# Optimization experiments

Measured on AMD Instinct MI355X. Metric: run time of the kernel, lower is better.

## Reference

```python
import jax, jax.numpy as jnp
import numpy as np

MARGIN = 1.0   # TripletLoss(margin) init arg
EPS = 1e-6     # torch F.pairwise_distance eps used by nn.TripletMarginLoss
INF = 1e9

N, D_EMB, N_CLASSES = 8192, 1024, 128


def setup_inputs() -> dict:
    key = jax.random.key(0)
    k1, k2 = jax.random.split(key)
    embeddings = jax.random.normal(k1, (N, D_EMB), dtype=jnp.float32)
    target = jax.random.randint(k2, (N,), 0, N_CLASSES, dtype=jnp.int64 if jax.config.jax_enable_x64 else jnp.int32)
    return {"embeddings": embeddings, "target": target}


def _mine_and_loss(embeddings, target):
    # Vectorized, deterministic equivalent of the per-anchor random mining loop:
    # full pairwise L2 distance matrix via a GEMM (compute-bound core).
    sq = jnp.sum(embeddings * embeddings, axis=1)                      # [N]
    d2 = sq[:, None] + sq[None, :] - 2.0 * (embeddings @ embeddings.T)  # [N, N]
    Dm = jnp.sqrt(jnp.maximum(d2, 0.0))                                 # [N, N]

    same = target[:, None] == target[None, :]
    eye = jnp.eye(target.shape[0], dtype=bool)
    pos_mask = same & ~eye          # valid positives (same class, not self)
    neg_mask = ~same                # valid negatives (different class)

    # Positive: hardest (farthest) same-class sample (deterministic stand-in
    # for the original's random positive draw).
    pos_scores = jnp.where(pos_mask, Dm, -INF)
    pos_idx = jnp.argmax(pos_scores, axis=1)                           # [N]
    d_p = jnp.max(pos_scores, axis=1)                                  # [N]

    # Negative: semi-hard (d_p < d_n < d_p + margin), pick the closest such
    # negative; if none exists, fall back to the overall hardest (min-dist)
    # negative -- mirrors the loop's early-break vs. min_dist fallback.
    semi = neg_mask & (Dm > d_p[:, None]) & (Dm < (d_p + MARGIN)[:, None])
    has_semi = jnp.any(semi, axis=1)
    neg_semi = jnp.argmin(jnp.where(semi, Dm, INF), axis=1)
    neg_hard = jnp.argmin(jnp.where(neg_mask, Dm, INF), axis=1)
    neg_idx = jnp.where(has_semi, neg_semi, neg_hard)                  # [N]

    # nn.TripletMarginLoss(margin, p=2): mean(relu(d(a,p) - d(a,n) + margin))
    # with torch's pairwise_distance eps added to the difference.
    a = embeddings
    p = embeddings[pos_idx]
    n = embeddings[neg_idx]
    dp = jnp.sqrt(jnp.sum((a - p + EPS) ** 2, axis=1))
    dn = jnp.sqrt(jnp.sum((a - n + EPS) ** 2, axis=1))
    return jnp.mean(jax.nn.relu(dp - dn + MARGIN))


def reference(embeddings, target):
    return _mine_and_loss(embeddings, target)
```

## Files before the change

### kernel.cpp

```cpp
#include <hip/hip_runtime.h>
#include <hip/hip_bf16.h>

#define N 8192
#define D 1024
#define MARGIN 1.0f
#define TSTR 132

typedef __attribute__((ext_vector_type(8))) short bf16x8;
typedef __attribute__((ext_vector_type(4))) float f32x4;
typedef __attribute__((ext_vector_type(8))) _Float16 f16x8;
typedef __attribute__((ext_vector_type(4))) _Float16 f16x4;
typedef __attribute__((ext_vector_type(8))) unsigned short u16x8;

__device__ inline unsigned short f2bf(float x) {
    unsigned u = __float_as_uint(x);
    unsigned r = (u + 0x7FFFu + ((u >> 16) & 1u)) >> 16;
    return (unsigned short)r;
}

__device__ inline float h2f(unsigned hb) {
    return (float)__builtin_bit_cast(_Float16, (unsigned short)(hb & 0xFFFFu));
}

__device__ inline void tri_decode(int l, int& a, int& b) {
    int bb = (int)((sqrtf(8.0f * (float)l + 1.0f) - 1.0f) * 0.5f);
    while ((bb + 1) * (bb + 2) / 2 <= l) ++bb;
    while (bb * (bb + 1) / 2 > l) --bb;
    b = bb;
    a = l - bb * (bb + 1) / 2;
}

__global__ __launch_bounds__(256) void prep_kernel(const float* __restrict__ E,
                                                   const int* __restrict__ target,
                                                   unsigned short* __restrict__ Ebf,
                                                   float* __restrict__ sq,
                                                   unsigned char* __restrict__ cls,
                                                   unsigned* __restrict__ P,
                                                   unsigned* __restrict__ Nn,
                                                   unsigned* __restrict__ S,
                                                   float* __restrict__ out) {
    const int r = blockIdx.x;
    const int tid = threadIdx.x;
    if (r < 32) {
        const int idx = r * 256 + tid;
        cls[idx] = (unsigned char)target[idx];
        P[idx] = 0u;
        Nn[idx] = 0xFFFFFFFFu;
        S[idx] = 0xFFFFFFFFu;
        if (idx == 0) out[0] = 0.0f;
    }
    const float4 v = ((const float4*)(E + (size_t)r * D))[tid];
    ushort4 o;
    o.x = f2bf(v.x); o.y = f2bf(v.y); o.z = f2bf(v.z); o.w = f2bf(v.w);
    ((ushort4*)(Ebf + (size_t)r * D))[tid] = o;
    float s = v.x * v.x + v.y * v.y + v.z * v.z + v.w * v.w;
    for (int off = 32; off > 0; off >>= 1) s += __shfl_down(s, off);
    __shared__ float red[4];
    const int lane = tid & 63, wave = tid >> 6;
    if (lane == 0) red[wave] = s;
    __syncthreads();
    if (tid == 0) sq[r] = red[0] + red[1] + red[2] + red[3];
}

__global__ __launch_bounds__(256) void gemm_kernel(const unsigned short* __restrict__ E,
                                                   const float* __restrict__ sq,
                                                   _Float16* __restrict__ D2h) {
    __shared__ char smem[128 * TSTR * 2];
    unsigned short* As = (unsigned short*)smem;
    unsigned short* Bs = (unsigned short*)(smem + 8192);
    _Float16* Ts = (_Float16*)smem;

    const int tid = threadIdx.x;
    const int lane = tid & 63;
    const int wave = tid >> 6;
    const int wm = wave & 1, wn = wave >> 1;

    int bx, by;
    tri_decode(blockIdx.x, bx, by);
    const int rm = by * 128;
    const int cn = bx * 128;

    const int srow = tid >> 2;
    const int rot_s = (srow >> 1) & 3;
    const int scol = (((tid & 3) + rot_s) & 3) * 8;

    const unsigned short* gA = E + (size_t)(rm + srow) * D + scol;
    const unsigned short* gB = E + (size_t)(cn + srow) * D + scol;

    f32x4 acc[4][4] = {};

    const int mr = lane & 15;
    const int kq2 = ((((lane >> 4)) - ((mr >> 1) & 3)) & 3) * 8;

    for (int k0 = 0; k0 < D; k0 += 32) {
        __builtin_amdgcn_global_load_lds(
            (const __attribute__((address_space(1))) unsigned int*)(gA + k0),
            (__attribute__((address_space(3))) unsigned int*)((char*)As + wave * 1024), 16, 0, 0);
        __builtin_amdgcn_global_load_lds(
            (const __attribute__((address_space(1))) unsigned int*)(gA + (size_t)64 * D + k0),
            (__attribute__((address_space(3))) unsigned int*)((char*)As + 4096 + wave * 1024), 16, 0, 0);
        __builtin_amdgcn_global_load_lds(
            (const __attribute__((address_space(1))) unsigned int*)(gB + k0),
            (__attribute__((address_space(3))) unsigned int*)((char*)Bs + wave * 1024), 16, 0, 0);
        __builtin_amdgcn_global_load_lds(
            (const __attribute__((address_space(1))) unsigned int*)(gB + (size_t)64 * D + k0),
            (__attribute__((address_space(3))) unsigned int*)((char*)Bs + 4096 + wave * 1024), 16, 0, 0);
        __syncthreads();

        bf16x8 af[4], bfr[4];
#pragma unroll
        for (int mi = 0; mi < 4; ++mi)
            af[mi] = *(const bf16x8*)(As + (wm * 64 + mi * 16 + mr) * 32 + kq2);
#pragma unroll
        for (int ni = 0; ni < 4; ++ni)
            bfr[ni] = *(const bf16x8*)(Bs + (wn * 64 + ni * 16 + mr) * 32 + kq2);
#pragma unroll
        for (int mi = 0; mi < 4; ++mi)
#pragma unroll
            for (int ni = 0; ni < 4; ++ni)
                acc[mi][ni] = __builtin_amdgcn_mfma_f32_16x16x32_bf16(af[mi], bfr[ni], acc[mi][ni], 0, 0, 0);
        __syncthreads();
    }

    const int crow = (lane >> 4) * 4;
    const int ccol = lane & 15;
    float sqj[4];
#pragma unroll
    for (int ni = 0; ni < 4; ++ni)
        sqj[ni] = sq[cn + wn * 64 + ni * 16 + ccol];
#pragma unroll
    for (int mi = 0; mi < 4; ++mi) {
        const int lrow = wm * 64 + mi * 16 + crow;
        const int i0 = rm + lrow;
        float sqi[4];
#pragma unroll
        for (int r = 0; r < 4; ++r) sqi[r] = sq[i0 + r];
#pragma unroll
        for (int ni = 0; ni < 4; ++ni) {
            const int lcol = wn * 64 + ni * 16 + ccol;
            f16x4 tv;
#pragma unroll
            for (int r = 0; r < 4; ++r) {
                float d2 = fmaxf(sqi[r] + sqj[ni] - 2.0f * acc[mi][ni][r], 0.0f);
                tv[r] = (_Float16)d2;
            }
            *(f16x4*)(Ts + (size_t)lcol * TSTR + lrow) = tv;
        }
    }
    __syncthreads();
#pragma unroll
    for (int it = 0; it < 8; ++it) {
        const int rt = it * 16 + (tid >> 4);
        const int seg = tid & 15;
        f16x4 v0 = *(const f16x4*)(Ts + (size_t)rt * TSTR + seg * 8);
        f16x4 v1 = *(const f16x4*)(Ts + (size_t)rt * TSTR + seg * 8 + 4);
        f16x8 v = __builtin_shufflevector(v0, v1, 0, 1, 2, 3, 4, 5, 6, 7);
        *(f16x8*)(D2h + (size_t)(cn + rt) * N + rm + seg * 8) = v;
    }
}

__global__ __launch_bounds__(256) void mineA_kernel(const _Float16* __restrict__ D2h,
                                                    const unsigned char* __restrict__ cls,
                                                    unsigned* __restrict__ P,
                                                    unsigned* __restrict__ Nn) {
    __shared__ unsigned char clsA_l[128], clsB_l[128];
    __shared__ unsigned short colP_l[4][128], colN_l[4][128];
    const int tid = threadIdx.x;
    const int lane = tid & 63, wave = tid >> 6;
    int a, b;
    tri_decode(blockIdx.x, a, b);
    if (tid < 128) clsA_l[tid] = cls[a * 128 + tid];
    else           clsB_l[tid - 128] = cls[b * 128 + (tid - 128)];
    __syncthreads();

    const int cg = tid & 15;
    const int rg = tid >> 4;
    const unsigned long long c8 = *(const unsigned long long*)(clsB_l + cg * 8);
    const unsigned short* g = (const unsigned short*)D2h + (size_t)(a * 128) * N + b * 128 + cg * 8;
    const bool offdiag = (a != b);

    unsigned cp[8], cnn[8];
#pragma unroll
    for (int e = 0; e < 8; ++e) { cp[e] = 0u; cnn[e] = 0xFFFFu; }

#pragma unroll
    for (int k = 0; k < 8; ++k) {
        const int r = k * 16 + rg;
        const unsigned rc = clsA_l[r];
        const u16x8 v = *(const u16x8*)(g + (size_t)r * N);
        unsigned rp = 0u, rn = 0xFFFFu;
#pragma unroll
        for (int e = 0; e < 8; ++e) {
            const unsigned hb = v[e];
            const bool s = (((unsigned)(c8 >> (8 * e)) & 0xFFu) == rc);
            rp = max(rp, s ? hb : 0u);
            rn = min(rn, s ? 0xFFFFu : hb);
            cp[e] = max(cp[e], s ? hb : 0u);
            cnn[e] = min(cnn[e], s ? 0xFFFFu : hb);
        }
#pragma unroll
        for (int m = 1; m < 16; m <<= 1) {
            rp = max(rp, (unsigned)__shfl_xor((int)rp, m));
            rn = min(rn, (unsigned)__shfl_xor((int)rn, m));
        }
        if (cg == 0) {
            atomicMax(&P[a * 128 + r], rp);
            atomicMin(&Nn[a * 128 + r], rn);
        }
    }
    if (offdiag) {
#pragma unroll
        for (int e = 0; e < 8; ++e) {
#pragma unroll
            for (int m = 16; m < 64; m <<= 1) {
                cp[e] = max(cp[e], (unsigned)__shfl_xor((int)cp[e], m));
                cnn[e] = min(cnn[e], (unsigned)__shfl_xor((int)cnn[e], m));
            }
        }
        if (lane < 16) {
#pragma unroll
            for (int e = 0; e < 8; ++e) {
                colP_l[wave][cg * 8 + e] = (unsigned short)cp[e];
                colN_l[wave][cg * 8 + e] = (unsigned short)cnn[e];
            }
        }
        __syncthreads();
        if (tid < 128) {
            const unsigned pm = max(max((unsigned)colP_l[0][tid], (unsigned)colP_l[1][tid]),
                                    max((unsigned)colP_l[2][tid], (unsigned)colP_l[3][tid]));
            const unsigned nm = min(min((unsigned)colN_l[0][tid], (unsigned)colN_l[1][tid]),
                                    min((unsigned)colN_l[2][tid], (unsigned)colN_l[3][tid]));
            atomicMax(&P[b * 128 + tid], pm);
            atomicMin(&Nn[b * 128 + tid], nm);
        }
    }
}

__global__ __launch_bounds__(256) void mineB_kernel(const _Float16* __restrict__ D2h,
                                                    const unsigned* __restrict__ P,
                                                    unsigned* __restrict__ S) {
    __shared__ unsigned short lobA_l[128], lobB_l[128];
    __shared__ unsigned short colS_l[4][128];
    const int tid = threadIdx.x;
    const int lane = tid & 63, wave = tid >> 6;
    int a, b;
    tri_decode(blockIdx.x, a, b);
    if (tid < 128) lobA_l[tid] = (unsigned short)P[a * 128 + tid];
    else           lobB_l[tid - 128] = (unsigned short)P[b * 128 + (tid - 128)];
    __syncthreads();

    const int cg = tid & 15;
    const int rg = tid >> 4;
    unsigned lb[8];
#pragma unroll
    for (int e = 0; e < 8; ++e) lb[e] = lobB_l[cg * 8 + e];
    const unsigned short* g = (const unsigned short*)D2h + (size_t)(a * 128) * N + b * 128 + cg * 8;
    const bool offdiag = (a != b);

    unsigned sc[8];
#pragma unroll
    for (int e = 0; e < 8; ++e) sc[e] = 0xFFFFu;

#pragma unroll
    for (int k = 0; k < 8; ++k) {
        const int r = k * 16 + rg;
        const unsigned lr = lobA_l[r];
        const u16x8 v = *(const u16x8*)(g + (size_t)r * N);
        unsigned sr = 0xFFFFu;
#pragma unroll
        for (int e = 0; e < 8; ++e) {
            const unsigned hb = v[e];
            sr = min(sr, hb > lr ? hb : 0xFFFFu);
            sc[e] = min(sc[e], hb > lb[e] ? hb : 0xFFFFu);
        }
#pragma unroll
        for (int m = 1; m < 16; m <<= 1)
            sr = min(sr, (unsigned)__shfl_xor((int)sr, m));
        if (cg == 0)
            atomicMin(&S[a * 128 + r], sr);
    }
    if (offdiag) {
#pragma unroll
        for (int e = 0; e < 8; ++e) {
#pragma unroll
            for (int m = 16; m < 64; m <<= 1)
                sc[e] = min(sc[e], (unsigned)__shfl_xor((int)sc[e], m));
        }
        if (lane < 16) {
#pragma unroll
            for (int e = 0; e < 8; ++e)
                colS_l[wave][cg * 8 + e] = (unsigned short)sc[e];
        }
        __syncthreads();
        if (tid < 128) {
            const unsigned sm = min(min((unsigned)colS_l[0][tid], (unsigned)colS_l[1][tid]),
                                    min((unsigned)colS_l[2][tid], (unsigned)colS_l[3][tid]));
            atomicMin(&S[b * 128 + tid], sm);
        }
    }
}

__global__ __launch_bounds__(256) void foldB_kernel(const unsigned* __restrict__ P,
                                                    const unsigned* __restrict__ Nn,
                                                    const unsigned* __restrict__ S,
                                                    float* __restrict__ out) {
    const int tid = threadIdx.x;
    const int i = blockIdx.x * 256 + tid;
    const float lo = h2f(P[i]);
    const float dp = sqrtf(lo);
    const float hw = dp + MARGIN;
    const float hi = hw * hw;
    const float smv = h2f(S[i]);
    const float dn2 = (smv < hi) ? smv : h2f(Nn[i]);
    float loss = fmaxf(dp - sqrtf(dn2) + MARGIN, 0.0f);
    for (int off = 32; off > 0; off >>= 1) loss += __shfl_down(loss, off);
    __shared__ float red[4];
    const int lane = tid & 63, wave = tid >> 6;
    if (lane == 0) red[wave] = loss;
    __syncthreads();
    if (tid == 0)
        atomicAdd(out, (red[0] + red[1] + red[2] + red[3]) * (1.0f / N));
}

extern "C" void kernel_launch(void* const* d_in, const int* in_sizes, int n_in,
                              void* d_out, int out_size, void* d_ws, size_t ws_size,
                              hipStream_t stream) {
    const float* E = (const float*)d_in[0];
    const int* target = (const int*)d_in[1];
    float* out = (float*)d_out;
    char* ws = (char*)d_ws;

    unsigned short* Ebf = (unsigned short*)ws;
    float* sq           = (float*)(ws + (size_t)16777216);
    unsigned char* cls  = (unsigned char*)(ws + (size_t)16809984);
    unsigned* P         = (unsigned*)(ws + (size_t)16842752);
    unsigned* Nn        = (unsigned*)(ws + (size_t)16875520);
    unsigned* S         = (unsigned*)(ws + (size_t)16908288);
    _Float16* D2h       = (_Float16*)(ws + (size_t)16941056);

    prep_kernel<<<N, 256, 0, stream>>>(E, target, Ebf, sq, cls, P, Nn, S, out);
    gemm_kernel<<<2080, 256, 0, stream>>>(Ebf, sq, D2h);
    mineA_kernel<<<2080, 256, 0, stream>>>(D2h, cls, P, Nn);
    mineB_kernel<<<2080, 256, 0, stream>>>(D2h, P, S);
    foldB_kernel<<<N / 256, 256, 0, stream>>>(P, Nn, S, out);
}
```

Baseline: 212.1 us.

## Fuse positive/hard-negative mining into GEMM epilogue and pack distance tiles

The first mining pass (hardest positive and hardest negative per row and column) now runs inside the GEMM epilogue on the register-resident fp16 distances, with per-block reductions through shared memory and atomics. This removes the separate mineA kernel and its full read of the distance matrix. Distance tiles are also stored contiguously per block instead of in the row-major N×N layout, so mineB reads them as one coalesced chunk. The cost is more epilogue work and register pressure in the GEMM, which could lower its occupancy.

```diff
diff --git a/kernel.cpp b/kernel.cpp
--- a/kernel.cpp
+++ b/kernel.cpp
@@ -64,11 +64,17 @@
 
 __global__ __launch_bounds__(256) void gemm_kernel(const unsigned short* __restrict__ E,
                                                    const float* __restrict__ sq,
-                                                   _Float16* __restrict__ D2h) {
+                                                   const unsigned char* __restrict__ cls,
+                                                   _Float16* __restrict__ D2pk,
+                                                   unsigned* __restrict__ P,
+                                                   unsigned* __restrict__ Nn) {
     __shared__ char smem[128 * TSTR * 2];
     unsigned short* As = (unsigned short*)smem;
     unsigned short* Bs = (unsigned short*)(smem + 8192);
     _Float16* Ts = (_Float16*)smem;
+    __shared__ unsigned char clr_l[128], clc_l[128];
+    __shared__ unsigned short rowP_l[256], rowN_l[256];
+    __shared__ unsigned short colP_l[256], colN_l[256];
 
     const int tid = threadIdx.x;
     const int lane = tid & 63;
@@ -79,6 +85,9 @@
     tri_decode(blockIdx.x, bx, by);
     const int rm = by * 128;
     const int cn = bx * 128;
+
+    if (tid < 128) clr_l[tid] = cls[rm + tid];
+    else           clc_l[tid - 128] = cls[cn + tid - 128];
 
     const int srow = tid >> 2;
     const int rot_s = (srow >> 1) & 3;
@@ -122,19 +131,31 @@
         __syncthreads();
     }
 
-    const int crow = (lane >> 4) * 4;
+    const int q = lane >> 4;
     const int ccol = lane & 15;
-    float sqj[4];
-#pragma unroll
-    for (int ni = 0; ni < 4; ++ni)
-        sqj[ni] = sq[cn + wn * 64 + ni * 16 + ccol];
+    const bool offdiag = (bx != by);
+
+    float sqj[4]; unsigned cj[4];
+#pragma unroll
+    for (int ni = 0; ni < 4; ++ni) {
+        const int lcol = wn * 64 + ni * 16 + ccol;
+        sqj[ni] = sq[cn + lcol];
+        cj[ni] = clc_l[lcol];
+    }
+
+    unsigned cp[4], cnn[4];
+#pragma unroll
+    for (int ni = 0; ni < 4; ++ni) { cp[ni] = 0u; cnn[ni] = 0xFFFFu; }
+
 #pragma unroll
     for (int mi = 0; mi < 4; ++mi) {
-        const int lrow = wm * 64 + mi * 16 + crow;
-        const int i0 = rm + lrow;
-        float sqi[4];
-#pragma unroll
-        for (int r = 0; r < 4; ++r) sqi[r] = sq[i0 + r];
+        const int lrow0 = wm * 64 + mi * 16 + q * 4;
+        float sqi[4]; unsigned ci[4];
+#pragma unroll
+        for (int r = 0; r < 4; ++r) { sqi[r] = sq[rm + lrow0 + r]; ci[r] = clr_l[lrow0 + r]; }
+        unsigned rp[4], rn[4];
+#pragma unroll
+        for (int r = 0; r < 4; ++r) { rp[r] = 0u; rn[r] = 0xFFFFu; }
 #pragma unroll
         for (int ni = 0; ni < 4; ++ni) {
             const int lcol = wn * 64 + ni * 16 + ccol;
@@ -142,12 +163,58 @@
 #pragma unroll
             for (int r = 0; r < 4; ++r) {
                 float d2 = fmaxf(sqi[r] + sqj[ni] - 2.0f * acc[mi][ni][r], 0.0f);
-                tv[r] = (_Float16)d2;
+                _Float16 h = (_Float16)d2;
+                tv[r] = h;
+                const unsigned hb = (unsigned)__builtin_bit_cast(unsigned short, h);
+                const bool s = (ci[r] == cj[ni]);
+                rp[r] = max(rp[r], s ? hb : 0u);
+                rn[r] = min(rn[r], s ? 0xFFFFu : hb);
+                cp[ni] = max(cp[ni], s ? hb : 0u);
+                cnn[ni] = min(cnn[ni], s ? 0xFFFFu : hb);
             }
-            *(f16x4*)(Ts + (size_t)lcol * TSTR + lrow) = tv;
+            *(f16x4*)(Ts + (size_t)lcol * TSTR + lrow0) = tv;
+        }
+#pragma unroll
+        for (int r = 0; r < 4; ++r) {
+#pragma unroll
+            for (int m = 1; m < 16; m <<= 1) {
+                rp[r] = max(rp[r], (unsigned)__shfl_xor((int)rp[r], m));
+                rn[r] = min(rn[r], (unsigned)__shfl_xor((int)rn[r], m));
+            }
+            if (ccol == 0) {
+                rowP_l[(lrow0 + r) * 2 + wn] = (unsigned short)rp[r];
+                rowN_l[(lrow0 + r) * 2 + wn] = (unsigned short)rn[r];
+            }
+        }
+    }
+#pragma unroll
+    for (int ni = 0; ni < 4; ++ni) {
+#pragma unroll
+        for (int m = 16; m < 64; m <<= 1) {
+            cp[ni] = max(cp[ni], (unsigned)__shfl_xor((int)cp[ni], m));
+            cnn[ni] = min(cnn[ni], (unsigned)__shfl_xor((int)cnn[ni], m));
+        }
+        if (q == 0) {
+            const int lcol = wn * 64 + ni * 16 + ccol;
+            colP_l[lcol * 2 + wm] = (unsigned short)cp[ni];
+            colN_l[lcol * 2 + wm] = (unsigned short)cnn[ni];
         }
     }
     __syncthreads();
+
+    if (tid < 128) {
+        const unsigned pm = max((unsigned)rowP_l[tid * 2], (unsigned)rowP_l[tid * 2 + 1]);
+        const unsigned nm = min((unsigned)rowN_l[tid * 2], (unsigned)rowN_l[tid * 2 + 1]);
+        atomicMax(&P[rm + tid], pm);
+        atomicMin(&Nn[rm + tid], nm);
+    } else if (offdiag) {
+        const int t = tid - 128;
+        const unsigned pm = max((unsigned)colP_l[t * 2], (unsigned)colP_l[t * 2 + 1]);
+        const unsigned nm = min((unsigned)colN_l[t * 2], (unsigned)colN_l[t * 2 + 1]);
+        atomicMax(&P[cn + t], pm);
+        atomicMin(&Nn[cn + t], nm);
+    }
+
 #pragma unroll
     for (int it = 0; it < 8; ++it) {
         const int rt = it * 16 + (tid >> 4);
@@ -155,88 +222,11 @@
         f16x4 v0 = *(const f16x4*)(Ts + (size_t)rt * TSTR + seg * 8);
         f16x4 v1 = *(const f16x4*)(Ts + (size_t)rt * TSTR + seg * 8 + 4);
         f16x8 v = __builtin_shufflevector(v0, v1, 0, 1, 2, 3, 4, 5, 6, 7);
-        *(f16x8*)(D2h + (size_t)(cn + rt) * N + rm + seg * 8) = v;
-    }
-}
-
-__global__ __launch_bounds__(256) void mineA_kernel(const _Float16* __restrict__ D2h,
-                                                    const unsigned char* __restrict__ cls,
-                                                    unsigned* __restrict__ P,
-                                                    unsigned* __restrict__ Nn) {
-    __shared__ unsigned char clsA_l[128], clsB_l[128];
-    __shared__ unsigned short colP_l[4][128], colN_l[4][128];
-    const int tid = threadIdx.x;
-    const int lane = tid & 63, wave = tid >> 6;
-    int a, b;
-    tri_decode(blockIdx.x, a, b);
-    if (tid < 128) clsA_l[tid] = cls[a * 128 + tid];
-    else           clsB_l[tid - 128] = cls[b * 128 + (tid - 128)];
-    __syncthreads();
-
-    const int cg = tid & 15;
-    const int rg = tid >> 4;
-    const unsigned long long c8 = *(const unsigned long long*)(clsB_l + cg * 8);
-    const unsigned short* g = (const unsigned short*)D2h + (size_t)(a * 128) * N + b * 128 + cg * 8;
-    const bool offdiag = (a != b);
-
-    unsigned cp[8], cnn[8];
-#pragma unroll
-    for (int e = 0; e < 8; ++e) { cp[e] = 0u; cnn[e] = 0xFFFFu; }
-
-#pragma unroll
-    for (int k = 0; k < 8; ++k) {
-        const int r = k * 16 + rg;
-        const unsigned rc = clsA_l[r];
-        const u16x8 v = *(const u16x8*)(g + (size_t)r * N);
-        unsigned rp = 0u, rn = 0xFFFFu;
-#pragma unroll
-        for (int e = 0; e < 8; ++e) {
-            const unsigned hb = v[e];
-            const bool s = (((unsigned)(c8 >> (8 * e)) & 0xFFu) == rc);
-            rp = max(rp, s ? hb : 0u);
-            rn = min(rn, s ? 0xFFFFu : hb);
-            cp[e] = max(cp[e], s ? hb : 0u);
-            cnn[e] = min(cnn[e], s ? 0xFFFFu : hb);
-        }
-#pragma unroll
-        for (int m = 1; m < 16; m <<= 1) {
-            rp = max(rp, (unsigned)__shfl_xor((int)rp, m));
-            rn = min(rn, (unsigned)__shfl_xor((int)rn, m));
-        }
-        if (cg == 0) {
-            atomicMax(&P[a * 128 + r], rp);
-            atomicMin(&Nn[a * 128 + r], rn);
-        }
-    }
-    if (offdiag) {
-#pragma unroll
-        for (int e = 0; e < 8; ++e) {
-#pragma unroll
-            for (int m = 16; m < 64; m <<= 1) {
-                cp[e] = max(cp[e], (unsigned)__shfl_xor((int)cp[e], m));
-                cnn[e] = min(cnn[e], (unsigned)__shfl_xor((int)cnn[e], m));
-            }
-        }
-        if (lane < 16) {
-#pragma unroll
-            for (int e = 0; e < 8; ++e) {
-                colP_l[wave][cg * 8 + e] = (unsigned short)cp[e];
-                colN_l[wave][cg * 8 + e] = (unsigned short)cnn[e];
-            }
-        }
-        __syncthreads();
-        if (tid < 128) {
-            const unsigned pm = max(max((unsigned)colP_l[0][tid], (unsigned)colP_l[1][tid]),
-                                    max((unsigned)colP_l[2][tid], (unsigned)colP_l[3][tid]));
-            const unsigned nm = min(min((unsigned)colN_l[0][tid], (unsigned)colN_l[1][tid]),
-                                    min((unsigned)colN_l[2][tid], (unsigned)colN_l[3][tid]));
-            atomicMax(&P[b * 128 + tid], pm);
-            atomicMin(&Nn[b * 128 + tid], nm);
-        }
-    }
-}
-
-__global__ __launch_bounds__(256) void mineB_kernel(const _Float16* __restrict__ D2h,
+        *(f16x8*)(D2pk + (size_t)blockIdx.x * 16384 + rt * 128 + seg * 8) = v;
+    }
+}
+
+__global__ __launch_bounds__(256) void mineB_kernel(const _Float16* __restrict__ D2pk,
                                                     const unsigned* __restrict__ P,
                                                     unsigned* __restrict__ S) {
     __shared__ unsigned short lobA_l[128], lobB_l[128];
@@ -250,11 +240,10 @@
     __syncthreads();
 
     const int cg = tid & 15;
-    const int rg = tid >> 4;
     unsigned lb[8];
 #pragma unroll
     for (int e = 0; e < 8; ++e) lb[e] = lobB_l[cg * 8 + e];
-    const unsigned short* g = (const unsigned short*)D2h + (size_t)(a * 128) * N + b * 128 + cg * 8;
+    const unsigned short* g = (const unsigned short*)D2pk + (size_t)blockIdx.x * 16384;
     const bool offdiag = (a != b);
 
     unsigned sc[8];
@@ -263,9 +252,9 @@
 
 #pragma unroll
     for (int k = 0; k < 8; ++k) {
-        const int r = k * 16 + rg;
+        const int r = k * 16 + (tid >> 4);
         const unsigned lr = lobA_l[r];
-        const u16x8 v = *(const u16x8*)(g + (size_t)r * N);
+        const u16x8 v = *(const u16x8*)(g + k * 2048 + tid * 8);
         unsigned sr = 0xFFFFu;
 #pragma unroll
         for (int e = 0; e < 8; ++e) {
@@ -336,11 +325,10 @@
     unsigned* P         = (unsigned*)(ws + (size_t)16842752);
     unsigned* Nn        = (unsigned*)(ws + (size_t)16875520);
     unsigned* S         = (unsigned*)(ws + (size_t)16908288);
-    _Float16* D2h       = (_Float16*)(ws + (size_t)16941056);
+    _Float16* D2pk      = (_Float16*)(ws + (size_t)16941056);
 
     prep_kernel<<<N, 256, 0, stream>>>(E, target, Ebf, sq, cls, P, Nn, S, out);
-    gemm_kernel<<<2080, 256, 0, stream>>>(Ebf, sq, D2h);
-    mineA_kernel<<<2080, 256, 0, stream>>>(D2h, cls, P, Nn);
-    mineB_kernel<<<2080, 256, 0, stream>>>(D2h, P, S);
+    gemm_kernel<<<2080, 256, 0, stream>>>(Ebf, sq, cls, D2pk, P, Nn);
+    mineB_kernel<<<2080, 256, 0, stream>>>(D2pk, P, S);
     foldB_kernel<<<N / 256, 256, 0, stream>>>(P, Nn, S, out);
 }
```

Result: slower. 231.0 us (+8.9%).

## Store distance tiles packed per block and replace atomics with partial buffers

Applied to the files above, without the earlier changes.

The GEMM now writes each 128x128 tile of the upper-triangular distance matrix contiguously per block instead of into a strided full N x N matrix, so the mining kernels read whole contiguous tiles. Per-row and per-column atomicMax/atomicMin on global arrays are replaced by writing per-tile partial maxima and minima into slab arrays (PR/PC/NR/NC/SR/SC). A new foldA kernel and an extended foldB kernel reduce those partials. This removes atomic contention and strided reads, at the cost of one extra kernel launch and extra partial-buffer traffic.

```diff
diff --git a/kernel.cpp b/kernel.cpp
--- a/kernel.cpp
+++ b/kernel.cpp
@@ -35,18 +35,12 @@
                                                    unsigned short* __restrict__ Ebf,
                                                    float* __restrict__ sq,
                                                    unsigned char* __restrict__ cls,
-                                                   unsigned* __restrict__ P,
-                                                   unsigned* __restrict__ Nn,
-                                                   unsigned* __restrict__ S,
                                                    float* __restrict__ out) {
     const int r = blockIdx.x;
     const int tid = threadIdx.x;
     if (r < 32) {
         const int idx = r * 256 + tid;
         cls[idx] = (unsigned char)target[idx];
-        P[idx] = 0u;
-        Nn[idx] = 0xFFFFFFFFu;
-        S[idx] = 0xFFFFFFFFu;
         if (idx == 0) out[0] = 0.0f;
     }
     const float4 v = ((const float4*)(E + (size_t)r * D))[tid];
@@ -64,7 +58,7 @@
 
 __global__ __launch_bounds__(256) void gemm_kernel(const unsigned short* __restrict__ E,
                                                    const float* __restrict__ sq,
-                                                   _Float16* __restrict__ D2h) {
+                                                   _Float16* __restrict__ D2pk) {
     __shared__ char smem[128 * TSTR * 2];
     unsigned short* As = (unsigned short*)smem;
     unsigned short* Bs = (unsigned short*)(smem + 8192);
@@ -155,15 +149,18 @@
         f16x4 v0 = *(const f16x4*)(Ts + (size_t)rt * TSTR + seg * 8);
         f16x4 v1 = *(const f16x4*)(Ts + (size_t)rt * TSTR + seg * 8 + 4);
         f16x8 v = __builtin_shufflevector(v0, v1, 0, 1, 2, 3, 4, 5, 6, 7);
-        *(f16x8*)(D2h + (size_t)(cn + rt) * N + rm + seg * 8) = v;
-    }
-}
-
-__global__ __launch_bounds__(256) void mineA_kernel(const _Float16* __restrict__ D2h,
+        *(f16x8*)(D2pk + (size_t)blockIdx.x * 16384 + rt * 128 + seg * 8) = v;
+    }
+}
+
+__global__ __launch_bounds__(256) void mineA_kernel(const _Float16* __restrict__ D2pk,
                                                     const unsigned char* __restrict__ cls,
-                                                    unsigned* __restrict__ P,
-                                                    unsigned* __restrict__ Nn) {
+                                                    unsigned short* __restrict__ PR,
+                                                    unsigned short* __restrict__ PC,
+                                                    unsigned short* __restrict__ NR,
+                                                    unsigned short* __restrict__ NC) {
     __shared__ unsigned char clsA_l[128], clsB_l[128];
+    __shared__ unsigned short rowP_l[128], rowN_l[128];
     __shared__ unsigned short colP_l[4][128], colN_l[4][128];
     const int tid = threadIdx.x;
     const int lane = tid & 63, wave = tid >> 6;
@@ -174,10 +171,8 @@
     __syncthreads();
 
     const int cg = tid & 15;
-    const int rg = tid >> 4;
     const unsigned long long c8 = *(const unsigned long long*)(clsB_l + cg * 8);
-    const unsigned short* g = (const unsigned short*)D2h + (size_t)(a * 128) * N + b * 128 + cg * 8;
-    const bool offdiag = (a != b);
+    const unsigned short* g = (const unsigned short*)D2pk + (size_t)blockIdx.x * 16384;
 
     unsigned cp[8], cnn[8];
 #pragma unroll
@@ -185,9 +180,9 @@
 
 #pragma unroll
     for (int k = 0; k < 8; ++k) {
-        const int r = k * 16 + rg;
+        const int r = k * 16 + (tid >> 4);
         const unsigned rc = clsA_l[r];
-        const u16x8 v = *(const u16x8*)(g + (size_t)r * N);
+        const u16x8 v = *(const u16x8*)(g + k * 2048 + tid * 8);
         unsigned rp = 0u, rn = 0xFFFFu;
 #pragma unroll
         for (int e = 0; e < 8; ++e) {
@@ -203,59 +198,77 @@
             rp = max(rp, (unsigned)__shfl_xor((int)rp, m));
             rn = min(rn, (unsigned)__shfl_xor((int)rn, m));
         }
-        if (cg == 0) {
-            atomicMax(&P[a * 128 + r], rp);
-            atomicMin(&Nn[a * 128 + r], rn);
-        }
-    }
-    if (offdiag) {
+        if (cg == 0) { rowP_l[r] = (unsigned short)rp; rowN_l[r] = (unsigned short)rn; }
+    }
+#pragma unroll
+    for (int e = 0; e < 8; ++e) {
+#pragma unroll
+        for (int m = 16; m < 64; m <<= 1) {
+            cp[e] = max(cp[e], (unsigned)__shfl_xor((int)cp[e], m));
+            cnn[e] = min(cnn[e], (unsigned)__shfl_xor((int)cnn[e], m));
+        }
+    }
+    if (lane < 16) {
 #pragma unroll
         for (int e = 0; e < 8; ++e) {
-#pragma unroll
-            for (int m = 16; m < 64; m <<= 1) {
-                cp[e] = max(cp[e], (unsigned)__shfl_xor((int)cp[e], m));
-                cnn[e] = min(cnn[e], (unsigned)__shfl_xor((int)cnn[e], m));
-            }
-        }
-        if (lane < 16) {
-#pragma unroll
-            for (int e = 0; e < 8; ++e) {
-                colP_l[wave][cg * 8 + e] = (unsigned short)cp[e];
-                colN_l[wave][cg * 8 + e] = (unsigned short)cnn[e];
-            }
-        }
-        __syncthreads();
-        if (tid < 128) {
-            const unsigned pm = max(max((unsigned)colP_l[0][tid], (unsigned)colP_l[1][tid]),
-                                    max((unsigned)colP_l[2][tid], (unsigned)colP_l[3][tid]));
-            const unsigned nm = min(min((unsigned)colN_l[0][tid], (unsigned)colN_l[1][tid]),
-                                    min((unsigned)colN_l[2][tid], (unsigned)colN_l[3][tid]));
-            atomicMax(&P[b * 128 + tid], pm);
-            atomicMin(&Nn[b * 128 + tid], nm);
-        }
-    }
-}
-
-__global__ __launch_bounds__(256) void mineB_kernel(const _Float16* __restrict__ D2h,
-                                                    const unsigned* __restrict__ P,
-                                                    unsigned* __restrict__ S) {
+            colP_l[wave][cg * 8 + e] = (unsigned short)cp[e];
+            colN_l[wave][cg * 8 + e] = (unsigned short)cnn[e];
+        }
+    }
+    __syncthreads();
+    if (tid < 128) {
+        PR[(size_t)b * N + a * 128 + tid] = rowP_l[tid];
+        NR[(size_t)b * N + a * 128 + tid] = rowN_l[tid];
+        const unsigned pm = max(max((unsigned)colP_l[0][tid], (unsigned)colP_l[1][tid]),
+                                max((unsigned)colP_l[2][tid], (unsigned)colP_l[3][tid]));
+        const unsigned nm = min(min((unsigned)colN_l[0][tid], (unsigned)colN_l[1][tid]),
+                                min((unsigned)colN_l[2][tid], (unsigned)colN_l[3][tid]));
+        PC[(size_t)a * N + b * 128 + tid] = (unsigned short)pm;
+        NC[(size_t)a * N + b * 128 + tid] = (unsigned short)nm;
+    }
+}
+
+__global__ __launch_bounds__(256) void foldA_kernel(const unsigned short* __restrict__ PR,
+                                                    const unsigned short* __restrict__ PC,
+                                                    const unsigned short* __restrict__ NR,
+                                                    const unsigned short* __restrict__ NC,
+                                                    unsigned short* __restrict__ P,
+                                                    unsigned short* __restrict__ Nn) {
+    const int i = blockIdx.x * 256 + threadIdx.x;
+    const int ai = i >> 7;
+    unsigned pm = 0u, nm = 0xFFFFu;
+    for (int s = ai; s < 64; ++s) {
+        pm = max(pm, (unsigned)PR[(size_t)s * N + i]);
+        nm = min(nm, (unsigned)NR[(size_t)s * N + i]);
+    }
+    for (int s = 0; s <= ai; ++s) {
+        pm = max(pm, (unsigned)PC[(size_t)s * N + i]);
+        nm = min(nm, (unsigned)NC[(size_t)s * N + i]);
+    }
+    P[i] = (unsigned short)pm;
+    Nn[i] = (unsigned short)nm;
+}
+
+__global__ __launch_bounds__(256) void mineB_kernel(const _Float16* __restrict__ D2pk,
+                                                    const unsigned short* __restrict__ P,
+                                                    unsigned short* __restrict__ SR,
+                                                    unsigned short* __restrict__ SC) {
     __shared__ unsigned short lobA_l[128], lobB_l[128];
+    __shared__ unsigned short rowS_l[128];
     __shared__ unsigned short colS_l[4][128];
     const int tid = threadIdx.x;
     const int lane = tid & 63, wave = tid >> 6;
     int a, b;
     tri_decode(blockIdx.x, a, b);
-    if (tid < 128) lobA_l[tid] = (unsigned short)P[a * 128 + tid];
-    else           lobB_l[tid - 128] = (unsigned short)P[b * 128 + (tid - 128)];
+    if (tid < 128) lobA_l[tid] = P[a * 128 + tid];
+    else           lobB_l[tid - 128] = P[b * 128 + (tid - 128)];
     __syncthreads();
 
     const int cg = tid & 15;
-    const int rg = tid >> 4;
     unsigned lb[8];
 #pragma unroll
     for (int e = 0; e < 8; ++e) lb[e] = lobB_l[cg * 8 + e];
-    const unsigned short* g = (const unsigned short*)D2h + (size_t)(a * 128) * N + b * 128 + cg * 8;
-    const bool offdiag = (a != b);
+    const unsigned short* g = (const unsigned short*)D2pk + (size_t)blockIdx.x * 16384;
 
     unsigned sc[8];
 #pragma unroll
@@ -263,9 +276,9 @@
 
 #pragma unroll
     for (int k = 0; k < 8; ++k) {
-        const int r = k * 16 + rg;
+        const int r = k * 16 + (tid >> 4);
         const unsigned lr = lobA_l[r];
-        const u16x8 v = *(const u16x8*)(g + (size_t)r * N);
+        const u16x8 v = *(const u16x8*)(g + k * 2048 + tid * 8);
         unsigned sr = 0xFFFFu;
 #pragma unroll
         for (int e = 0; e < 8; ++e) {
@@ -276,41 +289,44 @@
 #pragma unroll
         for (int m = 1; m < 16; m <<= 1)
             sr = min(sr, (unsigned)__shfl_xor((int)sr, m));
-        if (cg == 0)
-            atomicMin(&S[a * 128 + r], sr);
-    }
-    if (offdiag) {
-#pragma unroll
-        for (int e = 0; e < 8; ++e) {
-#pragma unroll
-            for (int m = 16; m < 64; m <<= 1)
-                sc[e] = min(sc[e], (unsigned)__shfl_xor((int)sc[e], m));
-        }
-        if (lane < 16) {
-#pragma unroll
-            for (int e = 0; e < 8; ++e)
-                colS_l[wave][cg * 8 + e] = (unsigned short)sc[e];
-        }
-        __syncthreads();
-        if (tid < 128) {
-            const unsigned sm = min(min((unsigned)colS_l[0][tid], (unsigned)colS_l[1][tid]),
-                                    min((unsigned)colS_l[2][tid], (unsigned)colS_l[3][tid]));
-            atomicMin(&S[b * 128 + tid], sm);
-        }
-    }
-}
-
-__global__ __launch_bounds__(256) void foldB_kernel(const unsigned* __restrict__ P,
-                                                    const unsigned* __restrict__ Nn,
-                                                    const unsigned* __restrict__ S,
+        if (cg == 0) rowS_l[r] = (unsigned short)sr;
+    }
+#pragma unroll
+    for (int e = 0; e < 8; ++e) {
+#pragma unroll
+        for (int m = 16; m < 64; m <<= 1)
+            sc[e] = min(sc[e], (unsigned)__shfl_xor((int)sc[e], m));
+    }
+    if (lane < 16) {
+#pragma unroll
+        for (int e = 0; e < 8; ++e)
+            colS_l[wave][cg * 8 + e] = (unsigned short)sc[e];
+    }
+    __syncthreads();
+    if (tid < 128) {
+        SR[(size_t)b * N + a * 128 + tid] = rowS_l[tid];
+        const unsigned sm = min(min((unsigned)colS_l[0][tid], (unsigned)colS_l[1][tid]),
+                                min((unsigned)colS_l[2][tid], (unsigned)colS_l[3][tid]));
+        SC[(size_t)a * N + b * 128 + tid] = (unsigned short)sm;
+    }
+}
+
+__global__ __launch_bounds__(256) void foldB_kernel(const unsigned short* __restrict__ SR,
+                                                    const unsigned short* __restrict__ SC,
+                                                    const unsigned short* __restrict__ P,
+                                                    const unsigned short* __restrict__ Nn,
                                                     float* __restrict__ out) {
     const int tid = threadIdx.x;
     const int i = blockIdx.x * 256 + tid;
+    const int ai = i >> 7;
+    unsigned sm = 0xFFFFu;
+    for (int s = ai; s < 64; ++s) sm = min(sm, (unsigned)SR[(size_t)s * N + i]);
+    for (int s = 0; s <= ai; ++s) sm = min(sm, (unsigned)SC[(size_t)s * N + i]);
     const float lo = h2f(P[i]);
     const float dp = sqrtf(lo);
     const float hw = dp + MARGIN;
     const float hi = hw * hw;
-    const float smv = h2f(S[i]);
+    const float smv = h2f(sm);
     const float dn2 = (smv < hi) ? smv : h2f(Nn[i]);
     float loss = fmaxf(dp - sqrtf(dn2) + MARGIN, 0.0f);
     for (int off = 32; off > 0; off >>= 1) loss += __shfl_down(loss, off);
@@ -333,14 +349,20 @@
     unsigned short* Ebf = (unsigned short*)ws;
     float* sq           = (float*)(ws + (size_t)16777216);
     unsigned char* cls  = (unsigned char*)(ws + (size_t)16809984);
-    unsigned* P         = (unsigned*)(ws + (size_t)16842752);
-    unsigned* Nn        = (unsigned*)(ws + (size_t)16875520);
-    unsigned* S         = (unsigned*)(ws + (size_t)16908288);
-    _Float16* D2h       = (_Float16*)(ws + (size_t)16941056);
-
-    prep_kernel<<<N, 256, 0, stream>>>(E, target, Ebf, sq, cls, P, Nn, S, out);
-    gemm_kernel<<<2080, 256, 0, stream>>>(Ebf, sq, D2h);
-    mineA_kernel<<<2080, 256, 0, stream>>>(D2h, cls, P, Nn);
-    mineB_kernel<<<2080, 256, 0, stream>>>(D2h, P, S);
-    foldB_kernel<<<N / 256, 256, 0, stream>>>(P, Nn, S, out);
-}
+    unsigned short* P   = (unsigned short*)(ws + (size_t)16842752);
+    unsigned short* Nn  = (unsigned short*)(ws + (size_t)16875520);
+    unsigned short* PR  = (unsigned short*)(ws + (size_t)16908288);
+    unsigned short* PC  = (unsigned short*)(ws + (size_t)17956864);
+    unsigned short* NR  = (unsigned short*)(ws + (size_t)19005440);
+    unsigned short* NC  = (unsigned short*)(ws + (size_t)20054016);
+    unsigned short* SR  = (unsigned short*)(ws + (size_t)21102592);
+    unsigned short* SC  = (unsigned short*)(ws + (size_t)22151168);
+    _Float16* D2pk      = (_Float16*)(ws + (size_t)23199744);
+
+    prep_kernel<<<N, 256, 0, stream>>>(E, target, Ebf, sq, cls, out);
+    gemm_kernel<<<2080, 256, 0, stream>>>(Ebf, sq, D2pk);
+    mineA_kernel<<<2080, 256, 0, stream>>>(D2pk, cls, PR, PC, NR, NC);
+    foldA_kernel<<<N / 256, 256, 0, stream>>>(PR, PC, NR, NC, P, Nn);
+    mineB_kernel<<<2080, 256, 0, stream>>>(D2pk, P, SR, SC);
+    foldB_kernel<<<N / 256, 256, 0, stream>>>(SR, SC, P, Nn, out);
+}
```

Result: slower. 226.8 us (+6.9%).
